# Kernel tuning notes

Hardware: AMD Instinct MI355X
Metric: run time of the kernel (lower is better)

The kernel has to match this reference:

```python
import jax, jax.numpy as jnp
import numpy as np

B, C, IMG, P = 64, 3, 224, 16
D, L, H, DH, M, NC = 768, 12, 12, 64, 3072, 1000
INNER = H * DH
PD = C * P * P          # patch_dim = 768
NP = (IMG // P) ** 2    # 196 patches


def setup_inputs() -> dict:
    key = jax.random.key(0)
    ks = jax.random.split(key, 16)
    s = 0.02
    nrm = lambda k, shape: jax.random.normal(k, shape, jnp.float32) * s
    return dict(
        img=jax.random.normal(ks[0], (B, C, IMG, IMG), jnp.float32),
        patch_ln1_g=jnp.ones(PD), patch_ln1_b=jnp.zeros(PD),
        patch_w=nrm(ks[1], (PD, D)), patch_b=jnp.zeros(D),
        patch_ln2_g=jnp.ones(D), patch_ln2_b=jnp.zeros(D),
        pos_emb=nrm(ks[2], (1, NP + 1, D)),
        cls_tok=nrm(ks[3], (1, 1, D)),
        attn_ln_g=jnp.ones((L, D)), attn_ln_b=jnp.zeros((L, D)),
        w_qkv=nrm(ks[4], (L, D, 3 * INNER)),
        w_out=nrm(ks[5], (L, INNER, D)), b_out=jnp.zeros((L, D)),
        ff_ln_g=jnp.ones((L, D)), ff_ln_b=jnp.zeros((L, D)),
        ff_w1=nrm(ks[6], (L, D, M)), ff_b1=jnp.zeros((L, M)),
        ff_w2=nrm(ks[7], (L, M, D)), ff_b2=jnp.zeros((L, D)),
        final_ln_g=jnp.ones(D), final_ln_b=jnp.zeros(D),
        head_w=nrm(ks[8], (D, NC)), head_b=jnp.zeros(NC),
    )


def _ln(x, g, b, eps=1e-5):
    m = x.mean(-1, keepdims=True)
    v = ((x - m) ** 2).mean(-1, keepdims=True)
    return (x - m) / jnp.sqrt(v + eps) * g + b


def reference(img, patch_ln1_g, patch_ln1_b, patch_w, patch_b, patch_ln2_g,
              patch_ln2_b, pos_emb, cls_tok, attn_ln_g, attn_ln_b, w_qkv,
              w_out, b_out, ff_ln_g, ff_ln_b, ff_w1, ff_b1, ff_w2, ff_b2,
              final_ln_g, final_ln_b, head_w, head_b):
    b, c, hh, ww = img.shape
    h, w = hh // P, ww // P
    # Rearrange 'b c (h p1) (w p2) -> b (h w) (p1 p2 c)'
    x = img.reshape(b, c, h, P, w, P).transpose(0, 2, 4, 3, 5, 1).reshape(b, h * w, P * P * c)
    x = _ln(x, patch_ln1_g, patch_ln1_b)
    x = x @ patch_w + patch_b
    x = _ln(x, patch_ln2_g, patch_ln2_b)
    n = x.shape[1]
    x = jnp.concatenate([jnp.broadcast_to(cls_tok, (b, 1, x.shape[-1])), x], axis=1)
    x = x + pos_emb[:, : n + 1]
    scale = DH ** -0.5
    for l in range(L):
        xn = _ln(x, attn_ln_g[l], attn_ln_b[l])
        qkv = xn @ w_qkv[l]  # [b, n+1, 3*inner]
        q, k, v = jnp.split(qkv, 3, axis=-1)
        sp = lambda t: t.reshape(b, -1, H, DH).transpose(0, 2, 1, 3)  # b h n d
        q, k, v = sp(q), sp(k), sp(v)
        # softmax variant: exp(scores*scale), normalize by sum + eps (no max-subtract, faithful to source)
        numer = jnp.exp(jnp.einsum('bhid,bhjd->bhij', q, k) * scale)
        attn = numer / (numer.sum(-1, keepdims=True) + 1e-8)
        out = jnp.einsum('bhij,bhjd->bhid', attn, v)
        out = out.transpose(0, 2, 1, 3).reshape(b, -1, INNER)
        x = out @ w_out[l] + b_out[l] + x
        xn = _ln(x, ff_ln_g[l], ff_ln_b[l])
        hid = jax.nn.gelu(xn @ ff_w1[l] + ff_b1[l], approximate=False)
        x = hid @ ff_w2[l] + ff_b2[l] + x
    x = _ln(x, final_ln_g, final_ln_b)
    return x[:, 0] @ head_w + head_b
```

## Files before the change

### kernel.cpp

```cpp
#include <hip/hip_runtime.h>
#include <hip/hip_bf16.h>
#include <math.h>

#define B_     64
#define NTOK   197
#define NPATCH 196
#define D768   768
#define NL     12
#define NH     12
#define MFF    3072
#define NCLS   1000
#define ROWS   (B_ * NTOK)
#define PROWS  (B_ * NPATCH)
#define ROWS_PAD 12672

typedef unsigned short ushort;
typedef __bf16 bf16x8 __attribute__((ext_vector_type(8)));
typedef float  f32x4  __attribute__((ext_vector_type(4)));
typedef unsigned short u16x4 __attribute__((ext_vector_type(4)));

__device__ __forceinline__ ushort f2b(float f) {
  __hip_bfloat16 h = __float2bfloat16(f);
  return *reinterpret_cast<ushort*>(&h);
}

__device__ __forceinline__ void gload16(const ushort* g, ushort* lds) {
  __builtin_amdgcn_global_load_lds((const __attribute__((address_space(1))) void*)g,
                                   (__attribute__((address_space(3))) void*)lds, 16, 0, 0);
}

__device__ __forceinline__ float gelu_f(float v) {
  float t = v * fmaf(0.0713548162726f, v * v, 1.5957691216f);
  return v / (1.0f + __expf(-t));
}

__device__ __forceinline__ void block_mean_rstd(float s, float sq, float& mean, float& rstd) {
#pragma unroll
  for (int off = 32; off; off >>= 1) { s += __shfl_xor(s, off); sq += __shfl_xor(sq, off); }
  __shared__ float ss[4], ssq[4];
  int w = threadIdx.x >> 6;
  if ((threadIdx.x & 63) == 0) { ss[w] = s; ssq[w] = sq; }
  __syncthreads();
  s  = ss[0] + ss[1] + ss[2] + ss[3];
  sq = ssq[0] + ssq[1] + ssq[2] + ssq[3];
  mean = s * (1.0f / 768.0f);
  float var = sq * (1.0f / 768.0f) - mean * mean;
  rstd = rsqrtf(var + 1e-5f);
}

__global__ __launch_bounds__(256) void ln_rows_b(const float* __restrict__ in, long in_stride,
                                                 const float* __restrict__ g,
                                                 const float* __restrict__ bta,
                                                 ushort* __restrict__ out) {
  const float* xr = in + (size_t)blockIdx.x * in_stride;
  int t = threadIdx.x;
  float v0 = xr[t], v1 = xr[t + 256], v2 = xr[t + 512];
  float mean, rstd;
  block_mean_rstd(v0 + v1 + v2, v0 * v0 + v1 * v1 + v2 * v2, mean, rstd);
  ushort* o = out + (size_t)blockIdx.x * 768;
  o[t]       = f2b((v0 - mean) * rstd * g[t]       + bta[t]);
  o[t + 256] = f2b((v1 - mean) * rstd * g[t + 256] + bta[t + 256]);
  o[t + 512] = f2b((v2 - mean) * rstd * g[t + 512] + bta[t + 512]);
}

__global__ __launch_bounds__(256) void patch_ln1(const float* __restrict__ img,
                                                 const float* __restrict__ g,
                                                 const float* __restrict__ bta,
                                                 ushort* __restrict__ xp) {
  int pidx = blockIdx.x;
  int b = pidx / NPATCH, hw = pidx % NPATCH;
  int ph = hw / 14, pw = hw % 14;
  int t = threadIdx.x;
  float v[3];
#pragma unroll
  for (int u = 0; u < 3; ++u) {
    int k = t + u * 256;
    int c = k % 3, p2 = (k / 3) & 15, p1 = k / 48;
    v[u] = img[(((size_t)b * 3 + c) * 224 + ph * 16 + p1) * 224 + pw * 16 + p2];
  }
  float mean, rstd;
  block_mean_rstd(v[0] + v[1] + v[2], v[0] * v[0] + v[1] * v[1] + v[2] * v[2], mean, rstd);
  ushort* o = xp + (size_t)pidx * 768;
#pragma unroll
  for (int u = 0; u < 3; ++u) { int k = t + u * 256; o[k] = f2b((v[u] - mean) * rstd * g[k] + bta[k]); }
}

__global__ __launch_bounds__(256) void ln2_pos(const float* __restrict__ xe,
                                               const float* __restrict__ g,
                                               const float* __restrict__ bta,
                                               const float* __restrict__ pos,
                                               float* __restrict__ x) {
  int pidx = blockIdx.x;
  int b = pidx / NPATCH, i = pidx % NPATCH;
  const float* xr = xe + (size_t)pidx * 768;
  int t = threadIdx.x;
  float v0 = xr[t], v1 = xr[t + 256], v2 = xr[t + 512];
  float mean, rstd;
  block_mean_rstd(v0 + v1 + v2, v0 * v0 + v1 * v1 + v2 * v2, mean, rstd);
  const float* p = pos + (size_t)(1 + i) * 768;
  float* o = x + ((size_t)b * NTOK + 1 + i) * 768;
  o[t]       = (v0 - mean) * rstd * g[t]       + bta[t]       + p[t];
  o[t + 256] = (v1 - mean) * rstd * g[t + 256] + bta[t + 256] + p[t + 256];
  o[t + 512] = (v2 - mean) * rstd * g[t + 512] + bta[t + 512] + p[t + 512];
}

__global__ __launch_bounds__(256) void cls_init(const float* __restrict__ cls_tok,
                                                const float* __restrict__ pos,
                                                float* __restrict__ x) {
  int b = blockIdx.x, t = threadIdx.x;
  float* o = x + (size_t)b * NTOK * 768;
#pragma unroll
  for (int u = 0; u < 3; ++u) { int k = t + u * 256; o[k] = cls_tok[k] + pos[k]; }
}

__global__ __launch_bounds__(256) void transpose_cast(const float* __restrict__ W,
                                                      ushort* __restrict__ Wt,
                                                      int K, int N) {
  __shared__ float t[32][33];
  int n0 = blockIdx.x * 32, k0 = blockIdx.y * 32;
  int tx = threadIdx.x, ty = threadIdx.y;
#pragma unroll
  for (int u = 0; u < 32; u += 8) {
    int n = n0 + tx;
    t[ty + u][tx] = (n < N) ? W[(size_t)(k0 + ty + u) * N + n] : 0.f;
  }
  __syncthreads();
#pragma unroll
  for (int u = 0; u < 32; u += 8) {
    int n = n0 + ty + u;
    if (n < N) Wt[(size_t)n * K + k0 + tx] = f2b(t[tx][ty + u]);
  }
}

__global__ __launch_bounds__(256) void transpose4(const float* __restrict__ wq,
                                                  const float* __restrict__ wo,
                                                  const float* __restrict__ w1,
                                                  const float* __restrict__ w2,
                                                  ushort* __restrict__ tq,
                                                  ushort* __restrict__ to,
                                                  ushort* __restrict__ t1,
                                                  ushort* __restrict__ t2) {
  int bid = blockIdx.x;
  const float* W; ushort* Wt; int K, N, xt;
  if (bid < 1728)      {             W = wq; Wt = tq; K = 768;  N = 2304; xt = 72; }
  else if (bid < 2304) { bid -= 1728; W = wo; Wt = to; K = 768;  N = 768;  xt = 24; }
  else if (bid < 4608) { bid -= 2304; W = w1; Wt = t1; K = 768;  N = 3072; xt = 96; }
  else                 { bid -= 4608; W = w2; Wt = t2; K = 3072; N = 768;  xt = 24; }
  int n0 = (bid % xt) * 32, k0 = (bid / xt) * 32;
  __shared__ float t[32][33];
  int tx = threadIdx.x, ty = threadIdx.y;
#pragma unroll
  for (int u = 0; u < 32; u += 8)
    t[ty + u][tx] = W[(size_t)(k0 + ty + u) * N + n0 + tx];
  __syncthreads();
#pragma unroll
  for (int u = 0; u < 32; u += 8)
    Wt[(size_t)(n0 + ty + u) * K + k0 + tx] = f2b(t[tx][ty + u]);
}

template<int EP, int RESID, int OBF>
__global__ __launch_bounds__(256, 4) void gemm_v6(const ushort* __restrict__ A,
                                                  const ushort* __restrict__ Bt,
                                                  const float* __restrict__ bias,
                                                  const float* __restrict__ resid,
                                                  void* __restrict__ Cv,
                                                  int M, int N, int K) {
  __shared__ ushort smem[2 * 8192];

  const int tid = threadIdx.x;
  const int w = tid >> 6, l = tid & 63;
  const int fr = l & 15, fc = l >> 4;

  const int ntx = gridDim.x;
  const int nwg = ntx * gridDim.y;
  const int orig = blockIdx.y * ntx + blockIdx.x;
  const int q = nwg >> 3, r = nwg & 7, xcd = orig & 7, idx = orig >> 3;
  const int wg = (xcd < r ? xcd * (q + 1) : r * (q + 1) + (xcd - r) * q) + idx;
  const int row0 = (wg / ntx) * 128, col0 = (wg % ntx) * 128;

  const int wr = (w >> 1) * 64, wc = (w & 1) * 64;

  const int srow = tid >> 2;
  const int sg = (tid & 3) ^ ((srow >> 1) & 3);
  const ushort* pA0 = A  + (size_t)(row0 + srow) * K + sg * 8;
  const ushort* pA1 = A  + (size_t)(row0 + 64 + srow) * K + sg * 8;
  const ushort* pB0 = Bt + (size_t)(col0 + srow) * K + sg * 8;
  const ushort* pB1 = Bt + (size_t)(col0 + 64 + srow) * K + sg * 8;

  auto stage = [&](int t_, ushort* dst) {
    const int k0 = t_ * 32;
    gload16(pA0 + k0, dst + tid * 8);
    gload16(pA1 + k0, dst + (tid + 256) * 8);
    gload16(pB0 + k0, dst + 4096 + tid * 8);
    gload16(pB1 + k0, dst + 4096 + (tid + 256) * 8);
  };

  int idxA[4], idxB[4];
#pragma unroll
  for (int m = 0; m < 4; ++m) {
    int rA = wr + m * 16 + fr;
    idxA[m] = rA * 32 + ((fc ^ ((rA >> 1) & 3)) << 3);
  }
#pragma unroll
  for (int n = 0; n < 4; ++n) {
    int rB = wc + n * 16 + fr;
    idxB[n] = rB * 32 + ((fc ^ ((rB >> 1) & 3)) << 3);
  }

  f32x4 acc[4][4] = {};

  auto compute = [&](const ushort* As) {
    const ushort* Bs = As + 4096;
    bf16x8 a_[4], b_[4];
#pragma unroll
    for (int m = 0; m < 4; ++m) a_[m] = *(const bf16x8*)(As + idxA[m]);
#pragma unroll
    for (int n = 0; n < 4; ++n) b_[n] = *(const bf16x8*)(Bs + idxB[n]);
#pragma unroll
    for (int m = 0; m < 4; ++m)
#pragma unroll
      for (int n = 0; n < 4; ++n)
        acc[m][n] = __builtin_amdgcn_mfma_f32_16x16x32_bf16(b_[n], a_[m], acc[m][n], 0, 0, 0);
  };

#define VM4() asm volatile("s_waitcnt vmcnt(4)" ::: "memory")
#define VM0() asm volatile("s_waitcnt vmcnt(0)" ::: "memory")

  const int NT = K >> 5;

  stage(0, smem);
  for (int t = 0; t < NT; t += 2) {
    if (t + 1 < NT) { stage(t + 1, smem + 8192); VM4(); } else VM0();
    __builtin_amdgcn_s_barrier();
    compute(smem);
    __builtin_amdgcn_s_barrier();
    if (t + 1 < NT) {
      if (t + 2 < NT) { stage(t + 2, smem); VM4(); } else VM0();
      __builtin_amdgcn_s_barrier();
      compute(smem + 8192);
      __builtin_amdgcn_s_barrier();
    }
  }
#undef VM4
#undef VM0

  if (!OBF) {
    float* Cf = (float*)Cv;
#pragma unroll
    for (int m = 0; m < 4; ++m) {
      int row = row0 + wr + m * 16 + fr;
      if (row >= M) continue;
#pragma unroll
      for (int n = 0; n < 4; ++n) {
        int col = col0 + wc + n * 16 + fc * 4;
        f32x4 v = acc[m][n];
        if (bias) v += *(const f32x4*)(bias + col);
        if (EP) {
#pragma unroll
          for (int rr = 0; rr < 4; ++rr) v[rr] = gelu_f(v[rr]);
        }
        if (RESID) v += *(const f32x4*)(resid + (size_t)row * N + col);
        *(f32x4*)(Cf + (size_t)row * N + col) = v;
      }
    }
  } else {
    __syncthreads();
    ushort* Cw = smem + w * 4096;
#pragma unroll
    for (int m = 0; m < 4; ++m) {
      int rl = m * 16 + fr;
#pragma unroll
      for (int n = 0; n < 4; ++n) {
        int col = col0 + wc + n * 16 + fc * 4;
        f32x4 v = acc[m][n];
        if (bias) v += *(const f32x4*)(bias + col);
        if (EP) {
#pragma unroll
          for (int rr = 0; rr < 4; ++rr) v[rr] = gelu_f(v[rr]);
        }
        u16x4 pk = { f2b(v[0]), f2b(v[1]), f2b(v[2]), f2b(v[3]) };
        int s = (n * 4 + fc) ^ (rl & 7);
        *(u16x4*)(Cw + rl * 64 + s * 4) = pk;
      }
    }
    ushort* Cb = (ushort*)Cv;
#pragma unroll
    for (int pp = 0; pp < 16; ++pp) {
      int rl = pp * 4 + (l >> 4);
      int cs = l & 15;
      u16x4 pk = *(const u16x4*)(Cw + rl * 64 + ((cs ^ (rl & 7)) * 4));
      int row = row0 + wr + rl;
      if (row < M) *(u16x4*)(Cb + (size_t)row * N + col0 + wc + cs * 4) = pk;
    }
  }
}

template<int EP, int RESID, int OBF>
__global__ __launch_bounds__(256) void gemm_bt(const ushort* __restrict__ A,
                                               const ushort* __restrict__ Bt,
                                               const float* __restrict__ bias,
                                               const float* __restrict__ resid,
                                               void* __restrict__ C,
                                               int M, int N, int K) {
  __shared__ ushort As[128 * 32];
  __shared__ ushort Bs[128 * 32];
  int tid = threadIdx.x;
  int w = tid >> 6, l = tid & 63;
  int fr = l & 15, fc = l >> 4;
  int row0 = blockIdx.y * 128, col0 = blockIdx.x * 128;
  int wr = (w >> 1) * 64, wc = (w & 1) * 64;

  int srow0 = w * 32 + (l >> 2);
  int srow1 = srow0 + 16;
  int sc0 = (((l & 3) ^ ((srow0 >> 1) & 3)) << 3);
  int sc1 = (((l & 3) ^ ((srow1 >> 1) & 3)) << 3);
  const ushort* ga0 = A  + (size_t)(row0 + srow0) * K + sc0;
  const ushort* ga1 = A  + (size_t)(row0 + srow1) * K + sc1;
  const ushort* gb0 = Bt + (size_t)(col0 + srow0) * K + sc0;
  const ushort* gb1 = Bt + (size_t)(col0 + srow1) * K + sc1;

  int idxA[4], idxB[4];
#pragma unroll
  for (int m = 0; m < 4; ++m) {
    int rA = wr + m * 16 + fr;
    idxA[m] = rA * 32 + ((fc ^ ((rA >> 1) & 3)) << 3);
  }
#pragma unroll
  for (int n = 0; n < 4; ++n) {
    int rB = wc + n * 16 + fr;
    idxB[n] = rB * 32 + ((fc ^ ((rB >> 1) & 3)) << 3);
  }

  f32x4 acc[4][4] = {};

  for (int k0 = 0; k0 < K; k0 += 32) {
    gload16(ga0 + k0, &As[w * 1024]);
    gload16(ga1 + k0, &As[w * 1024 + 512]);
    gload16(gb0 + k0, &Bs[w * 1024]);
    gload16(gb1 + k0, &Bs[w * 1024 + 512]);
    __syncthreads();
    bf16x8 af[4], bfr[4];
#pragma unroll
    for (int m = 0; m < 4; ++m) af[m] = *(const bf16x8*)(As + idxA[m]);
#pragma unroll
    for (int n = 0; n < 4; ++n) bfr[n] = *(const bf16x8*)(Bs + idxB[n]);
#pragma unroll
    for (int m = 0; m < 4; ++m)
#pragma unroll
      for (int n = 0; n < 4; ++n)
        acc[m][n] = __builtin_amdgcn_mfma_f32_16x16x32_bf16(af[m], bfr[n], acc[m][n], 0, 0, 0);
    __syncthreads();
  }

#pragma unroll
  for (int n = 0; n < 4; ++n) {
    int col = col0 + wc + n * 16 + fr;
    if (col >= N) continue;
    float bv = bias ? bias[col] : 0.f;
#pragma unroll
    for (int m = 0; m < 4; ++m) {
#pragma unroll
      for (int rr = 0; rr < 4; ++rr) {
        int row = row0 + wr + m * 16 + fc * 4 + rr;
        if (row >= M) continue;
        float v = acc[m][n][rr] + bv;
        if (EP == 1) v = 0.5f * v * (1.0f + erff(v * 0.70710678118654752f));
        if (RESID) v += resid[(size_t)row * N + col];
        if (OBF) ((ushort*)C)[(size_t)row * N + col] = f2b(v);
        else     ((float*)C)[(size_t)row * N + col]  = v;
      }
    }
  }
}

__global__ __launch_bounds__(256) void attn_mfma(const ushort* __restrict__ qkv,
                                                 ushort* __restrict__ aout) {
  int bid = blockIdx.x;
  int qt = bid & 3;
  int h  = (bid >> 2) % NH;
  int b  = (bid >> 2) / NH;
  int tid = threadIdx.x, w = tid >> 6, l = tid & 63;
  int fr = l & 15, fc = l >> 4;

  __shared__ ushort Vt[64 * 64];
  __shared__ ushort Pl[4 * 16 * 64];

  const size_t brow = (size_t)b * NTOK;
  int q0 = qt * 64 + w * 16;

  bf16x8 qf[2];
  {
    const ushort* qp = qkv + (brow + q0 + fr) * 2304 + h * 64 + fc * 8;
    qf[0] = *(const bf16x8*)qp;
    qf[1] = *(const bf16x8*)(qp + 32);
  }
  float rs[4] = {0.f, 0.f, 0.f, 0.f};
  f32x4 oc[4] = {};

  for (int kt = 0; kt < 4; ++kt) {
    __syncthreads();
    {
      int key = tid >> 2, d0 = (tid & 3) * 16;
      int j = kt * 64 + key;
      bool valid = j < NTOK;
      const ushort* vp = qkv + (brow + j) * 2304 + 1536 + h * 64 + d0;
      ushort vbuf[16];
      if (valid) {
        *(bf16x8*)(vbuf)     = *(const bf16x8*)vp;
        *(bf16x8*)(vbuf + 8) = *(const bf16x8*)(vp + 8);
      } else {
#pragma unroll
        for (int i = 0; i < 16; ++i) vbuf[i] = 0;
      }
#pragma unroll
      for (int i = 0; i < 16; ++i) {
        int d = d0 + i;
        int byte = d * 128 + ((((key >> 3)) ^ (d & 7)) << 4) + (key & 7) * 2;
        Vt[byte >> 1] = vbuf[i];
      }
    }
    f32x4 sc[4];
#pragma unroll
    for (int n = 0; n < 4; ++n) {
      f32x4 z = {};
      const ushort* kp = qkv + (brow + kt * 64 + n * 16 + fr) * 2304 + 768 + h * 64 + fc * 8;
      bf16x8 k0 = *(const bf16x8*)kp;
      bf16x8 k1 = *(const bf16x8*)(kp + 32);
      z = __builtin_amdgcn_mfma_f32_16x16x32_bf16(qf[0], k0, z, 0, 0, 0);
      z = __builtin_amdgcn_mfma_f32_16x16x32_bf16(qf[1], k1, z, 0, 0, 0);
      sc[n] = z;
    }
    float part[4] = {0.f, 0.f, 0.f, 0.f};
#pragma unroll
    for (int n = 0; n < 4; ++n) {
      int j = kt * 64 + n * 16 + fr;
      bool jv = j < NTOK;
#pragma unroll
      for (int rr = 0; rr < 4; ++rr) {
        float e = jv ? __expf(sc[n][rr] * 0.125f) : 0.f;
        part[rr] += e;
        int row = fc * 4 + rr, col = n * 16 + fr;
        int byte = row * 128 + (((col >> 3) ^ (row & 7)) << 4) + (col & 7) * 2;
        Pl[w * 1024 + (byte >> 1)] = f2b(e);
      }
    }
#pragma unroll
    for (int rr = 0; rr < 4; ++rr) {
      float p = part[rr];
      p += __shfl_xor(p, 1); p += __shfl_xor(p, 2);
      p += __shfl_xor(p, 4); p += __shfl_xor(p, 8);
      rs[rr] += p;
    }
    __syncthreads();
#pragma unroll
    for (int ks = 0; ks < 2; ++ks) {
      int prow = fr;
      int pbyte = prow * 128 + (((ks * 4 + fc) ^ (prow & 7)) << 4);
      bf16x8 pf = *(const bf16x8*)(Pl + w * 1024 + (pbyte >> 1));
#pragma unroll
      for (int n = 0; n < 4; ++n) {
        int d = n * 16 + fr;
        int vb = d * 128 + (((ks * 4 + fc) ^ (d & 7)) << 4);
        bf16x8 vf = *(const bf16x8*)(Vt + (vb >> 1));
        oc[n] = __builtin_amdgcn_mfma_f32_16x16x32_bf16(pf, vf, oc[n], 0, 0, 0);
      }
    }
  }
#pragma unroll
  for (int n = 0; n < 4; ++n) {
#pragma unroll
    for (int rr = 0; rr < 4; ++rr) {
      int qq = q0 + fc * 4 + rr;
      if (qq < NTOK) {
        float v = oc[n][rr] / (rs[rr] + 1e-8f);
        aout[(brow + qq) * 768 + h * 64 + n * 16 + fr] = f2b(v);
      }
    }
  }
}

extern "C" void kernel_launch(void* const* d_in, const int* in_sizes, int n_in,
                              void* d_out, int out_size, void* d_ws, size_t ws_size,
                              hipStream_t stream) {
  const float* img       = (const float*)d_in[0];
  const float* p_ln1_g   = (const float*)d_in[1];
  const float* p_ln1_b   = (const float*)d_in[2];
  const float* patch_w   = (const float*)d_in[3];
  const float* patch_b   = (const float*)d_in[4];
  const float* p_ln2_g   = (const float*)d_in[5];
  const float* p_ln2_b   = (const float*)d_in[6];
  const float* pos_emb   = (const float*)d_in[7];
  const float* cls_tok   = (const float*)d_in[8];
  const float* attn_ln_g = (const float*)d_in[9];
  const float* attn_ln_b = (const float*)d_in[10];
  const float* w_qkv     = (const float*)d_in[11];
  const float* w_out     = (const float*)d_in[12];
  const float* b_out     = (const float*)d_in[13];
  const float* ff_ln_g   = (const float*)d_in[14];
  const float* ff_ln_b   = (const float*)d_in[15];
  const float* ff_w1     = (const float*)d_in[16];
  const float* ff_b1     = (const float*)d_in[17];
  const float* ff_w2     = (const float*)d_in[18];
  const float* ff_b2     = (const float*)d_in[19];
  const float* fin_ln_g  = (const float*)d_in[20];
  const float* fin_ln_b  = (const float*)d_in[21];
  const float* head_w    = (const float*)d_in[22];
  const float* head_b    = (const float*)d_in[23];
  float* out = (float*)d_out;

  char* p = (char*)d_ws;
  auto alloc = [&](size_t bytes) { char* r = p; p += (bytes + 255) & ~(size_t)255; return r; };
  float*  x      = (float*) alloc((size_t)ROWS_PAD * 768 * 4);
  ushort* xnb    = (ushort*)alloc((size_t)ROWS_PAD * 768 * 2);
  ushort* qkvb   = (ushort*)alloc((size_t)ROWS_PAD * 2304 * 2);
  ushort* aoutb  = (ushort*)alloc((size_t)ROWS_PAD * 768 * 2);
  ushort* wtq    = (ushort*)alloc((size_t)2304 * 768 * 2);
  ushort* wto    = (ushort*)alloc((size_t)768 * 768 * 2);
  ushort* wt1    = (ushort*)alloc((size_t)3072 * 768 * 2);
  ushort* wt2    = (ushort*)alloc((size_t)768 * 3072 * 2);
  ushort* pwt    = (ushort*)alloc((size_t)768 * 768 * 2);
  ushort* hwt    = (ushort*)alloc((size_t)1024 * 768 * 2);
  ushort* xclsb  = (ushort*)alloc((size_t)128 * 768 * 2);
  ushort* hidb   = qkvb;
  ushort* xpb    = xnb;
  float*  xe     = (float*)qkvb;

  dim3 blk(256), tblk(32, 8);

  transpose_cast<<<dim3(24, 24), tblk, 0, stream>>>(patch_w, pwt, 768, 768);
  transpose_cast<<<dim3(32, 24), tblk, 0, stream>>>(head_w, hwt, 768, 1000);
  patch_ln1<<<PROWS, blk, 0, stream>>>(img, p_ln1_g, p_ln1_b, xpb);
  gemm_v6<0, 0, 0><<<dim3(6, 98), blk, 0, stream>>>(xpb, pwt, patch_b, nullptr, xe,
                                                    PROWS, 768, 768);
  ln2_pos<<<PROWS, blk, 0, stream>>>(xe, p_ln2_g, p_ln2_b, pos_emb, x);
  cls_init<<<B_, blk, 0, stream>>>(cls_tok, pos_emb, x);

  for (int l = 0; l < NL; ++l) {
    transpose4<<<6912, tblk, 0, stream>>>(w_qkv + (size_t)l * 768 * 2304,
                                          w_out + (size_t)l * 768 * 768,
                                          ff_w1 + (size_t)l * 768 * MFF,
                                          ff_w2 + (size_t)l * MFF * 768,
                                          wtq, wto, wt1, wt2);

    ln_rows_b<<<ROWS, blk, 0, stream>>>(x, 768, attn_ln_g + (size_t)l * 768,
                                        attn_ln_b + (size_t)l * 768, xnb);
    gemm_v6<0, 0, 1><<<dim3(18, 99), blk, 0, stream>>>(xnb, wtq, nullptr, nullptr, qkvb,
                                                       ROWS, 2304, 768);
    attn_mfma<<<B_ * NH * 4, blk, 0, stream>>>(qkvb, aoutb);
    gemm_v6<0, 1, 0><<<dim3(6, 99), blk, 0, stream>>>(aoutb, wto, b_out + (size_t)l * 768,
                                                      x, x, ROWS, 768, 768);
    ln_rows_b<<<ROWS, blk, 0, stream>>>(x, 768, ff_ln_g + (size_t)l * 768,
                                        ff_ln_b + (size_t)l * 768, xnb);
    gemm_v6<1, 0, 1><<<dim3(24, 99), blk, 0, stream>>>(xnb, wt1, ff_b1 + (size_t)l * MFF,
                                                       nullptr, hidb, ROWS, MFF, 768);
    gemm_v6<0, 1, 0><<<dim3(6, 99), blk, 0, stream>>>(hidb, wt2, ff_b2 + (size_t)l * 768,
                                                      x, x, ROWS, 768, MFF);
  }

  ln_rows_b<<<B_, blk, 0, stream>>>(x, (long)NTOK * 768, fin_ln_g, fin_ln_b, xclsb);
  gemm_bt<0, 0, 0><<<dim3(8, 1), blk, 0, stream>>>(xclsb, hwt, head_b, nullptr, out,
                                                   B_, NCLS, 768);
}
```

Measured before the change: 4.344 ms.

## Widen GEMM tiles to 128x256 and pre-transpose all layer weights once

```diff
diff --git a/kernel.cpp b/kernel.cpp
--- a/kernel.cpp
+++ b/kernel.cpp
@@ -132,6 +132,28 @@
   }
 }
 
+__device__ __forceinline__ void transpose_layer(int bid,
+                                                const float* wq, const float* wo,
+                                                const float* w1, const float* w2,
+                                                ushort* tq, ushort* to,
+                                                ushort* t1, ushort* t2) {
+  const float* W; ushort* Wt; int K, N, xt;
+  if (bid < 1728)      {             W = wq; Wt = tq; K = 768;  N = 2304; xt = 72; }
+  else if (bid < 2304) { bid -= 1728; W = wo; Wt = to; K = 768;  N = 768;  xt = 24; }
+  else if (bid < 4608) { bid -= 2304; W = w1; Wt = t1; K = 768;  N = 3072; xt = 96; }
+  else                 { bid -= 4608; W = w2; Wt = t2; K = 3072; N = 768;  xt = 24; }
+  int n0 = (bid % xt) * 32, k0 = (bid / xt) * 32;
+  __shared__ float t[32][33];
+  int tx = threadIdx.x, ty = threadIdx.y;
+#pragma unroll
+  for (int u = 0; u < 32; u += 8)
+    t[ty + u][tx] = W[(size_t)(k0 + ty + u) * N + n0 + tx];
+  __syncthreads();
+#pragma unroll
+  for (int u = 0; u < 32; u += 8)
+    Wt[(size_t)(n0 + ty + u) * K + k0 + tx] = f2b(t[tx][ty + u]);
+}
+
 __global__ __launch_bounds__(256) void transpose4(const float* __restrict__ wq,
                                                   const float* __restrict__ wo,
                                                   const float* __restrict__ w1,
@@ -140,32 +162,33 @@
                                                   ushort* __restrict__ to,
                                                   ushort* __restrict__ t1,
                                                   ushort* __restrict__ t2) {
-  int bid = blockIdx.x;
-  const float* W; ushort* Wt; int K, N, xt;
-  if (bid < 1728)      {             W = wq; Wt = tq; K = 768;  N = 2304; xt = 72; }
-  else if (bid < 2304) { bid -= 1728; W = wo; Wt = to; K = 768;  N = 768;  xt = 24; }
-  else if (bid < 4608) { bid -= 2304; W = w1; Wt = t1; K = 768;  N = 3072; xt = 96; }
-  else                 { bid -= 4608; W = w2; Wt = t2; K = 3072; N = 768;  xt = 24; }
-  int n0 = (bid % xt) * 32, k0 = (bid / xt) * 32;
-  __shared__ float t[32][33];
-  int tx = threadIdx.x, ty = threadIdx.y;
-#pragma unroll
-  for (int u = 0; u < 32; u += 8)
-    t[ty + u][tx] = W[(size_t)(k0 + ty + u) * N + n0 + tx];
-  __syncthreads();
-#pragma unroll
-  for (int u = 0; u < 32; u += 8)
-    Wt[(size_t)(n0 + ty + u) * K + k0 + tx] = f2b(t[tx][ty + u]);
+  transpose_layer(blockIdx.x, wq, wo, w1, w2, tq, to, t1, t2);
+}
+
+__global__ __launch_bounds__(256) void transpose_all(const float* __restrict__ wq,
+                                                     const float* __restrict__ wo,
+                                                     const float* __restrict__ w1,
+                                                     const float* __restrict__ w2,
+                                                     ushort* __restrict__ tq,
+                                                     ushort* __restrict__ to,
+                                                     ushort* __restrict__ t1,
+                                                     ushort* __restrict__ t2) {
+  int l = blockIdx.x / 6912, bid = blockIdx.x % 6912;
+  transpose_layer(bid,
+                  wq + (size_t)l * 768 * 2304, wo + (size_t)l * 768 * 768,
+                  w1 + (size_t)l * 768 * MFF,  w2 + (size_t)l * MFF * 768,
+                  tq + (size_t)l * 2304 * 768, to + (size_t)l * 768 * 768,
+                  t1 + (size_t)l * MFF * 768,  t2 + (size_t)l * 768 * MFF);
 }
 
 template<int EP, int RESID, int OBF>
-__global__ __launch_bounds__(256, 4) void gemm_v6(const ushort* __restrict__ A,
+__global__ __launch_bounds__(256, 2) void gemm_v7(const ushort* __restrict__ A,
                                                   const ushort* __restrict__ Bt,
                                                   const float* __restrict__ bias,
                                                   const float* __restrict__ resid,
                                                   void* __restrict__ Cv,
                                                   int M, int N, int K) {
-  __shared__ ushort smem[2 * 8192];
+  __shared__ ushort smem[2 * 12288];
 
   const int tid = threadIdx.x;
   const int w = tid >> 6, l = tid & 63;
@@ -176,9 +199,9 @@
   const int orig = blockIdx.y * ntx + blockIdx.x;
   const int q = nwg >> 3, r = nwg & 7, xcd = orig & 7, idx = orig >> 3;
   const int wg = (xcd < r ? xcd * (q + 1) : r * (q + 1) + (xcd - r) * q) + idx;
-  const int row0 = (wg / ntx) * 128, col0 = (wg % ntx) * 128;
-
-  const int wr = (w >> 1) * 64, wc = (w & 1) * 64;
+  const int row0 = (wg / ntx) * 128, col0 = (wg % ntx) * 256;
+
+  const int wrow = (w >> 1) * 64, wcol = (w & 1) * 128;
 
   const int srow = tid >> 2;
   const int sg = (tid & 3) ^ ((srow >> 1) & 3);
@@ -186,73 +209,78 @@
   const ushort* pA1 = A  + (size_t)(row0 + 64 + srow) * K + sg * 8;
   const ushort* pB0 = Bt + (size_t)(col0 + srow) * K + sg * 8;
   const ushort* pB1 = Bt + (size_t)(col0 + 64 + srow) * K + sg * 8;
+  const ushort* pB2 = Bt + (size_t)(col0 + 128 + srow) * K + sg * 8;
+  const ushort* pB3 = Bt + (size_t)(col0 + 192 + srow) * K + sg * 8;
 
   auto stage = [&](int t_, ushort* dst) {
     const int k0 = t_ * 32;
     gload16(pA0 + k0, dst + tid * 8);
     gload16(pA1 + k0, dst + (tid + 256) * 8);
-    gload16(pB0 + k0, dst + 4096 + tid * 8);
-    gload16(pB1 + k0, dst + 4096 + (tid + 256) * 8);
+    ushort* db = dst + 4096;
+    gload16(pB0 + k0, db + tid * 8);
+    gload16(pB1 + k0, db + (tid + 256) * 8);
+    gload16(pB2 + k0, db + (tid + 512) * 8);
+    gload16(pB3 + k0, db + (tid + 768) * 8);
   };
 
-  int idxA[4], idxB[4];
+  int idxA[4], idxB[8];
 #pragma unroll
   for (int m = 0; m < 4; ++m) {
-    int rA = wr + m * 16 + fr;
+    int rA = wrow + m * 16 + fr;
     idxA[m] = rA * 32 + ((fc ^ ((rA >> 1) & 3)) << 3);
   }
 #pragma unroll
-  for (int n = 0; n < 4; ++n) {
-    int rB = wc + n * 16 + fr;
+  for (int n = 0; n < 8; ++n) {
+    int rB = wcol + n * 16 + fr;
     idxB[n] = rB * 32 + ((fc ^ ((rB >> 1) & 3)) << 3);
   }
 
-  f32x4 acc[4][4] = {};
+  f32x4 acc[4][8] = {};
 
   auto compute = [&](const ushort* As) {
     const ushort* Bs = As + 4096;
-    bf16x8 a_[4], b_[4];
+    bf16x8 a_[4], b_[8];
 #pragma unroll
     for (int m = 0; m < 4; ++m) a_[m] = *(const bf16x8*)(As + idxA[m]);
 #pragma unroll
-    for (int n = 0; n < 4; ++n) b_[n] = *(const bf16x8*)(Bs + idxB[n]);
+    for (int n = 0; n < 8; ++n) b_[n] = *(const bf16x8*)(Bs + idxB[n]);
 #pragma unroll
     for (int m = 0; m < 4; ++m)
 #pragma unroll
-      for (int n = 0; n < 4; ++n)
+      for (int n = 0; n < 8; ++n)
         acc[m][n] = __builtin_amdgcn_mfma_f32_16x16x32_bf16(b_[n], a_[m], acc[m][n], 0, 0, 0);
   };
 
-#define VM4() asm volatile("s_waitcnt vmcnt(4)" ::: "memory")
+#define VM6() asm volatile("s_waitcnt vmcnt(6)" ::: "memory")
 #define VM0() asm volatile("s_waitcnt vmcnt(0)" ::: "memory")
 
   const int NT = K >> 5;
 
   stage(0, smem);
   for (int t = 0; t < NT; t += 2) {
-    if (t + 1 < NT) { stage(t + 1, smem + 8192); VM4(); } else VM0();
+    if (t + 1 < NT) { stage(t + 1, smem + 12288); VM6(); } else VM0();
     __builtin_amdgcn_s_barrier();
     compute(smem);
     __builtin_amdgcn_s_barrier();
     if (t + 1 < NT) {
-      if (t + 2 < NT) { stage(t + 2, smem); VM4(); } else VM0();
+      if (t + 2 < NT) { stage(t + 2, smem); VM6(); } else VM0();
       __builtin_amdgcn_s_barrier();
-      compute(smem + 8192);
+      compute(smem + 12288);
       __builtin_amdgcn_s_barrier();
     }
   }
-#undef VM4
+#undef VM6
 #undef VM0
 
   if (!OBF) {
     float* Cf = (float*)Cv;
 #pragma unroll
     for (int m = 0; m < 4; ++m) {
-      int row = row0 + wr + m * 16 + fr;
+      int row = row0 + wrow + m * 16 + fr;
       if (row >= M) continue;
 #pragma unroll
-      for (int n = 0; n < 4; ++n) {
-        int col = col0 + wc + n * 16 + fc * 4;
+      for (int n = 0; n < 8; ++n) {
+        int col = col0 + wcol + n * 16 + fc * 4;
         f32x4 v = acc[m][n];
         if (bias) v += *(const f32x4*)(bias + col);
         if (EP) {
@@ -264,33 +292,38 @@
       }
     }
   } else {
-    __syncthreads();
     ushort* Cw = smem + w * 4096;
-#pragma unroll
-    for (int m = 0; m < 4; ++m) {
-      int rl = m * 16 + fr;
-#pragma unroll
-      for (int n = 0; n < 4; ++n) {
-        int col = col0 + wc + n * 16 + fc * 4;
-        f32x4 v = acc[m][n];
-        if (bias) v += *(const f32x4*)(bias + col);
-        if (EP) {
-#pragma unroll
-          for (int rr = 0; rr < 4; ++rr) v[rr] = gelu_f(v[rr]);
+    ushort* Cb = (ushort*)Cv;
+#pragma unroll
+    for (int mp = 0; mp < 2; ++mp) {
+#pragma unroll
+      for (int m2 = 0; m2 < 2; ++m2) {
+        int m = mp * 2 + m2;
+        int rl = m2 * 16 + fr;
+#pragma unroll
+        for (int n = 0; n < 8; ++n) {
+          int col = col0 + wcol + n * 16 + fc * 4;
+          f32x4 v = acc[m][n];
+          if (bias) v += *(const f32x4*)(bias + col);
+          if (EP) {
+#pragma unroll
+            for (int rr = 0; rr < 4; ++rr) v[rr] = gelu_f(v[rr]);
+          }
+          u16x4 pk = { f2b(v[0]), f2b(v[1]), f2b(v[2]), f2b(v[3]) };
+          int s = (n * 4 + fc) ^ (rl & 7);
+          *(u16x4*)(Cw + rl * 128 + s * 4) = pk;
         }
-        u16x4 pk = { f2b(v[0]), f2b(v[1]), f2b(v[2]), f2b(v[3]) };
-        int s = (n * 4 + fc) ^ (rl & 7);
-        *(u16x4*)(Cw + rl * 64 + s * 4) = pk;
-      }
-    }
-    ushort* Cb = (ushort*)Cv;
-#pragma unroll
-    for (int pp = 0; pp < 16; ++pp) {
-      int rl = pp * 4 + (l >> 4);
-      int cs = l & 15;
-      u16x4 pk = *(const u16x4*)(Cw + rl * 64 + ((cs ^ (rl & 7)) * 4));
-      int row = row0 + wr + rl;
-      if (row < M) *(u16x4*)(Cb + (size_t)row * N + col0 + wc + cs * 4) = pk;
+      }
+      asm volatile("s_waitcnt lgkmcnt(0)" ::: "memory");
+#pragma unroll
+      for (int pp = 0; pp < 16; ++pp) {
+        int rl = pp * 2 + (l >> 5);
+        int cs = l & 31;
+        u16x4 pk = *(const u16x4*)(Cw + rl * 128 + ((cs ^ (rl & 7)) * 4));
+        int row = row0 + wrow + mp * 32 + rl;
+        if (row < M) *(u16x4*)(Cb + (size_t)row * N + col0 + wcol + cs * 4) = pk;
+      }
+      asm volatile("s_waitcnt lgkmcnt(0)" ::: "memory");
     }
   }
 }
@@ -514,10 +547,6 @@
   ushort* xnb    = (ushort*)alloc((size_t)ROWS_PAD * 768 * 2);
   ushort* qkvb   = (ushort*)alloc((size_t)ROWS_PAD * 2304 * 2);
   ushort* aoutb  = (ushort*)alloc((size_t)ROWS_PAD * 768 * 2);
-  ushort* wtq    = (ushort*)alloc((size_t)2304 * 768 * 2);
-  ushort* wto    = (ushort*)alloc((size_t)768 * 768 * 2);
-  ushort* wt1    = (ushort*)alloc((size_t)3072 * 768 * 2);
-  ushort* wt2    = (ushort*)alloc((size_t)768 * 3072 * 2);
   ushort* pwt    = (ushort*)alloc((size_t)768 * 768 * 2);
   ushort* hwt    = (ushort*)alloc((size_t)1024 * 768 * 2);
   ushort* xclsb  = (ushort*)alloc((size_t)128 * 768 * 2);
@@ -525,35 +554,52 @@
   ushort* xpb    = xnb;
   float*  xe     = (float*)qkvb;
 
+  const size_t SQ = (size_t)2304 * 768, SO = (size_t)768 * 768, S1 = (size_t)MFF * 768;
+  size_t used = (size_t)(p - (char*)d_ws);
+  bool oneshot = (used + 12 * (SQ + SO + 2 * S1) * 2 + 4096) <= ws_size;
+  int nw = oneshot ? 12 : 1;
+  ushort* wtq = (ushort*)alloc(nw * SQ * 2);
+  ushort* wto = (ushort*)alloc(nw * SO * 2);
+  ushort* wt1 = (ushort*)alloc(nw * S1 * 2);
+  ushort* wt2 = (ushort*)alloc(nw * S1 * 2);
+
   dim3 blk(256), tblk(32, 8);
 
   transpose_cast<<<dim3(24, 24), tblk, 0, stream>>>(patch_w, pwt, 768, 768);
   transpose_cast<<<dim3(32, 24), tblk, 0, stream>>>(head_w, hwt, 768, 1000);
+  if (oneshot)
+    transpose_all<<<12 * 6912, tblk, 0, stream>>>(w_qkv, w_out, ff_w1, ff_w2,
+                                                  wtq, wto, wt1, wt2);
   patch_ln1<<<PROWS, blk, 0, stream>>>(img, p_ln1_g, p_ln1_b, xpb);
-  gemm_v6<0, 0, 0><<<dim3(6, 98), blk, 0, stream>>>(xpb, pwt, patch_b, nullptr, xe,
+  gemm_v7<0, 0, 0><<<dim3(3, 98), blk, 0, stream>>>(xpb, pwt, patch_b, nullptr, xe,
                                                     PROWS, 768, 768);
   ln2_pos<<<PROWS, blk, 0, stream>>>(xe, p_ln2_g, p_ln2_b, pos_emb, x);
   cls_init<<<B_, blk, 0, stream>>>(cls_tok, pos_emb, x);
 
   for (int l = 0; l < NL; ++l) {
-    transpose4<<<6912, tblk, 0, stream>>>(w_qkv + (size_t)l * 768 * 2304,
-                                          w_out + (size_t)l * 768 * 768,
-                                          ff_w1 + (size_t)l * 768 * MFF,
-                                          ff_w2 + (size_t)l * MFF * 768,
-                                          wtq, wto, wt1, wt2);
+    ushort* tq = wtq + (oneshot ? (size_t)l * SQ : 0);
+    ushort* to = wto + (oneshot ? (size_t)l * SO : 0);
+    ushort* t1 = wt1 + (oneshot ? (size_t)l * S1 : 0);
+    ushort* t2 = wt2 + (oneshot ? (size_t)l * S1 : 0);
+    if (!oneshot)
+      transpose4<<<6912, tblk, 0, stream>>>(w_qkv + (size_t)l * 768 * 2304,
+                                            w_out + (size_t)l * 768 * 768,
+                                            ff_w1 + (size_t)l * 768 * MFF,
+                                            ff_w2 + (size_t)l * MFF * 768,
+                                            tq, to, t1, t2);
 
     ln_rows_b<<<ROWS, blk, 0, stream>>>(x, 768, attn_ln_g + (size_t)l * 768,
                                         attn_ln_b + (size_t)l * 768, xnb);
-    gemm_v6<0, 0, 1><<<dim3(18, 99), blk, 0, stream>>>(xnb, wtq, nullptr, nullptr, qkvb,
-                                                       ROWS, 2304, 768);
+    gemm_v7<0, 0, 1><<<dim3(9, 99), blk, 0, stream>>>(xnb, tq, nullptr, nullptr, qkvb,
+                                                      ROWS, 2304, 768);
     attn_mfma<<<B_ * NH * 4, blk, 0, stream>>>(qkvb, aoutb);
-    gemm_v6<0, 1, 0><<<dim3(6, 99), blk, 0, stream>>>(aoutb, wto, b_out + (size_t)l * 768,
+    gemm_v7<0, 1, 0><<<dim3(3, 99), blk, 0, stream>>>(aoutb, to, b_out + (size_t)l * 768,
                                                       x, x, ROWS, 768, 768);
     ln_rows_b<<<ROWS, blk, 0, stream>>>(x, 768, ff_ln_g + (size_t)l * 768,
                                         ff_ln_b + (size_t)l * 768, xnb);
-    gemm_v6<1, 0, 1><<<dim3(24, 99), blk, 0, stream>>>(xnb, wt1, ff_b1 + (size_t)l * MFF,
+    gemm_v7<1, 0, 1><<<dim3(12, 99), blk, 0, stream>>>(xnb, t1, ff_b1 + (size_t)l * MFF,
                                                        nullptr, hidb, ROWS, MFF, 768);
-    gemm_v6<0, 1, 0><<<dim3(6, 99), blk, 0, stream>>>(hidb, wt2, ff_b2 + (size_t)l * 768,
+    gemm_v7<0, 1, 0><<<dim3(3, 99), blk, 0, stream>>>(hidb, t2, ff_b2 + (size_t)l * 768,
                                                       x, x, ROWS, 768, MFF);
   }
 
```

Result: slower. 4.612 ms (+6.2%).

## Store residual stream in bf16 and pre-transpose all layer weights in one launch

Applied to the files above, without the earlier changes.

```diff
diff --git a/kernel.cpp b/kernel.cpp
--- a/kernel.cpp
+++ b/kernel.cpp
@@ -23,6 +23,12 @@
   __hip_bfloat16 h = __float2bfloat16(f);
   return *reinterpret_cast<ushort*>(&h);
 }
+__device__ __forceinline__ float b2f(ushort u) {
+  unsigned int v = ((unsigned int)u) << 16;
+  float f;
+  __builtin_memcpy(&f, &v, 4);
+  return f;
+}
 
 __device__ __forceinline__ void gload16(const ushort* g, ushort* lds) {
   __builtin_amdgcn_global_load_lds((const __attribute__((address_space(1))) void*)g,
@@ -48,13 +54,13 @@
   rstd = rsqrtf(var + 1e-5f);
 }
 
-__global__ __launch_bounds__(256) void ln_rows_b(const float* __restrict__ in, long in_stride,
+__global__ __launch_bounds__(256) void ln_rows_b(const ushort* __restrict__ in, long in_stride,
                                                  const float* __restrict__ g,
                                                  const float* __restrict__ bta,
                                                  ushort* __restrict__ out) {
-  const float* xr = in + (size_t)blockIdx.x * in_stride;
+  const ushort* xr = in + (size_t)blockIdx.x * in_stride;
   int t = threadIdx.x;
-  float v0 = xr[t], v1 = xr[t + 256], v2 = xr[t + 512];
+  float v0 = b2f(xr[t]), v1 = b2f(xr[t + 256]), v2 = b2f(xr[t + 512]);
   float mean, rstd;
   block_mean_rstd(v0 + v1 + v2, v0 * v0 + v1 * v1 + v2 * v2, mean, rstd);
   ushort* o = out + (size_t)blockIdx.x * 768;
@@ -89,7 +95,7 @@
                                                const float* __restrict__ g,
                                                const float* __restrict__ bta,
                                                const float* __restrict__ pos,
-                                               float* __restrict__ x) {
+                                               ushort* __restrict__ x) {
   int pidx = blockIdx.x;
   int b = pidx / NPATCH, i = pidx % NPATCH;
   const float* xr = xe + (size_t)pidx * 768;
@@ -98,19 +104,19 @@
   float mean, rstd;
   block_mean_rstd(v0 + v1 + v2, v0 * v0 + v1 * v1 + v2 * v2, mean, rstd);
   const float* p = pos + (size_t)(1 + i) * 768;
-  float* o = x + ((size_t)b * NTOK + 1 + i) * 768;
-  o[t]       = (v0 - mean) * rstd * g[t]       + bta[t]       + p[t];
-  o[t + 256] = (v1 - mean) * rstd * g[t + 256] + bta[t + 256] + p[t + 256];
-  o[t + 512] = (v2 - mean) * rstd * g[t + 512] + bta[t + 512] + p[t + 512];
+  ushort* o = x + ((size_t)b * NTOK + 1 + i) * 768;
+  o[t]       = f2b((v0 - mean) * rstd * g[t]       + bta[t]       + p[t]);
+  o[t + 256] = f2b((v1 - mean) * rstd * g[t + 256] + bta[t + 256] + p[t + 256]);
+  o[t + 512] = f2b((v2 - mean) * rstd * g[t + 512] + bta[t + 512] + p[t + 512]);
 }
 
 __global__ __launch_bounds__(256) void cls_init(const float* __restrict__ cls_tok,
                                                 const float* __restrict__ pos,
-                                                float* __restrict__ x) {
+                                                ushort* __restrict__ x) {
   int b = blockIdx.x, t = threadIdx.x;
-  float* o = x + (size_t)b * NTOK * 768;
-#pragma unroll
-  for (int u = 0; u < 3; ++u) { int k = t + u * 256; o[k] = cls_tok[k] + pos[k]; }
+  ushort* o = x + (size_t)b * NTOK * 768;
+#pragma unroll
+  for (int u = 0; u < 3; ++u) { int k = t + u * 256; o[k] = f2b(cls_tok[k] + pos[k]); }
 }
 
 __global__ __launch_bounds__(256) void transpose_cast(const float* __restrict__ W,
@@ -130,6 +136,28 @@
     int n = n0 + ty + u;
     if (n < N) Wt[(size_t)n * K + k0 + tx] = f2b(t[tx][ty + u]);
   }
+}
+
+__device__ __forceinline__ void transpose_layer(int bid,
+                                                const float* wq, const float* wo,
+                                                const float* w1, const float* w2,
+                                                ushort* tq, ushort* to,
+                                                ushort* t1, ushort* t2) {
+  const float* W; ushort* Wt; int K, N, xt;
+  if (bid < 1728)      {             W = wq; Wt = tq; K = 768;  N = 2304; xt = 72; }
+  else if (bid < 2304) { bid -= 1728; W = wo; Wt = to; K = 768;  N = 768;  xt = 24; }
+  else if (bid < 4608) { bid -= 2304; W = w1; Wt = t1; K = 768;  N = 3072; xt = 96; }
+  else                 { bid -= 4608; W = w2; Wt = t2; K = 3072; N = 768;  xt = 24; }
+  int n0 = (bid % xt) * 32, k0 = (bid / xt) * 32;
+  __shared__ float t[32][33];
+  int tx = threadIdx.x, ty = threadIdx.y;
+#pragma unroll
+  for (int u = 0; u < 32; u += 8)
+    t[ty + u][tx] = W[(size_t)(k0 + ty + u) * N + n0 + tx];
+  __syncthreads();
+#pragma unroll
+  for (int u = 0; u < 32; u += 8)
+    Wt[(size_t)(n0 + ty + u) * K + k0 + tx] = f2b(t[tx][ty + u]);
 }
 
 __global__ __launch_bounds__(256) void transpose4(const float* __restrict__ wq,
@@ -140,29 +168,30 @@
                                                   ushort* __restrict__ to,
                                                   ushort* __restrict__ t1,
                                                   ushort* __restrict__ t2) {
-  int bid = blockIdx.x;
-  const float* W; ushort* Wt; int K, N, xt;
-  if (bid < 1728)      {             W = wq; Wt = tq; K = 768;  N = 2304; xt = 72; }
-  else if (bid < 2304) { bid -= 1728; W = wo; Wt = to; K = 768;  N = 768;  xt = 24; }
-  else if (bid < 4608) { bid -= 2304; W = w1; Wt = t1; K = 768;  N = 3072; xt = 96; }
-  else                 { bid -= 4608; W = w2; Wt = t2; K = 3072; N = 768;  xt = 24; }
-  int n0 = (bid % xt) * 32, k0 = (bid / xt) * 32;
-  __shared__ float t[32][33];
-  int tx = threadIdx.x, ty = threadIdx.y;
-#pragma unroll
-  for (int u = 0; u < 32; u += 8)
-    t[ty + u][tx] = W[(size_t)(k0 + ty + u) * N + n0 + tx];
-  __syncthreads();
-#pragma unroll
-  for (int u = 0; u < 32; u += 8)
-    Wt[(size_t)(n0 + ty + u) * K + k0 + tx] = f2b(t[tx][ty + u]);
+  transpose_layer(blockIdx.x, wq, wo, w1, w2, tq, to, t1, t2);
+}
+
+__global__ __launch_bounds__(256) void transpose_all(const float* __restrict__ wq,
+                                                     const float* __restrict__ wo,
+                                                     const float* __restrict__ w1,
+                                                     const float* __restrict__ w2,
+                                                     ushort* __restrict__ tq,
+                                                     ushort* __restrict__ to,
+                                                     ushort* __restrict__ t1,
+                                                     ushort* __restrict__ t2) {
+  int l = blockIdx.x / 6912, bid = blockIdx.x % 6912;
+  transpose_layer(bid,
+                  wq + (size_t)l * 768 * 2304, wo + (size_t)l * 768 * 768,
+                  w1 + (size_t)l * 768 * MFF,  w2 + (size_t)l * MFF * 768,
+                  tq + (size_t)l * 2304 * 768, to + (size_t)l * 768 * 768,
+                  t1 + (size_t)l * MFF * 768,  t2 + (size_t)l * 768 * MFF);
 }
 
 template<int EP, int RESID, int OBF>
 __global__ __launch_bounds__(256, 4) void gemm_v6(const ushort* __restrict__ A,
                                                   const ushort* __restrict__ Bt,
                                                   const float* __restrict__ bias,
-                                                  const float* __restrict__ resid,
+                                                  const void* __restrict__ resid,
                                                   void* __restrict__ Cv,
                                                   int M, int N, int K) {
   __shared__ ushort smem[2 * 8192];
@@ -259,7 +288,7 @@
 #pragma unroll
           for (int rr = 0; rr < 4; ++rr) v[rr] = gelu_f(v[rr]);
         }
-        if (RESID) v += *(const f32x4*)(resid + (size_t)row * N + col);
+        if (RESID) v += *(const f32x4*)((const float*)resid + (size_t)row * N + col);
         *(f32x4*)(Cf + (size_t)row * N + col) = v;
       }
     }
@@ -269,6 +298,7 @@
 #pragma unroll
     for (int m = 0; m < 4; ++m) {
       int rl = m * 16 + fr;
+      int row = row0 + wr + rl;
 #pragma unroll
       for (int n = 0; n < 4; ++n) {
         int col = col0 + wc + n * 16 + fc * 4;
@@ -277,6 +307,11 @@
         if (EP) {
 #pragma unroll
           for (int rr = 0; rr < 4; ++rr) v[rr] = gelu_f(v[rr]);
+        }
+        if (RESID) {
+          u16x4 rv = *(const u16x4*)((const ushort*)resid + (size_t)row * N + col);
+#pragma unroll
+          for (int rr = 0; rr < 4; ++rr) v[rr] += b2f(rv[rr]);
         }
         u16x4 pk = { f2b(v[0]), f2b(v[1]), f2b(v[2]), f2b(v[3]) };
         int s = (n * 4 + fc) ^ (rl & 7);
@@ -510,14 +545,10 @@
 
   char* p = (char*)d_ws;
   auto alloc = [&](size_t bytes) { char* r = p; p += (bytes + 255) & ~(size_t)255; return r; };
-  float*  x      = (float*) alloc((size_t)ROWS_PAD * 768 * 4);
+  ushort* x      = (ushort*)alloc((size_t)ROWS_PAD * 768 * 2);
   ushort* xnb    = (ushort*)alloc((size_t)ROWS_PAD * 768 * 2);
   ushort* qkvb   = (ushort*)alloc((size_t)ROWS_PAD * 2304 * 2);
   ushort* aoutb  = (ushort*)alloc((size_t)ROWS_PAD * 768 * 2);
-  ushort* wtq    = (ushort*)alloc((size_t)2304 * 768 * 2);
-  ushort* wto    = (ushort*)alloc((size_t)768 * 768 * 2);
-  ushort* wt1    = (ushort*)alloc((size_t)3072 * 768 * 2);
-  ushort* wt2    = (ushort*)alloc((size_t)768 * 3072 * 2);
   ushort* pwt    = (ushort*)alloc((size_t)768 * 768 * 2);
   ushort* hwt    = (ushort*)alloc((size_t)1024 * 768 * 2);
   ushort* xclsb  = (ushort*)alloc((size_t)128 * 768 * 2);
@@ -525,10 +556,22 @@
   ushort* xpb    = xnb;
   float*  xe     = (float*)qkvb;
 
+  const size_t SQ = (size_t)2304 * 768, SO = (size_t)768 * 768, S1 = (size_t)MFF * 768;
+  size_t used = (size_t)(p - (char*)d_ws);
+  bool oneshot = (used + 12 * (SQ + SO + 2 * S1) * 2 + 4096) <= ws_size;
+  int nw = oneshot ? 12 : 1;
+  ushort* wtq = (ushort*)alloc(nw * SQ * 2);
+  ushort* wto = (ushort*)alloc(nw * SO * 2);
+  ushort* wt1 = (ushort*)alloc(nw * S1 * 2);
+  ushort* wt2 = (ushort*)alloc(nw * S1 * 2);
+
   dim3 blk(256), tblk(32, 8);
 
   transpose_cast<<<dim3(24, 24), tblk, 0, stream>>>(patch_w, pwt, 768, 768);
   transpose_cast<<<dim3(32, 24), tblk, 0, stream>>>(head_w, hwt, 768, 1000);
+  if (oneshot)
+    transpose_all<<<12 * 6912, tblk, 0, stream>>>(w_qkv, w_out, ff_w1, ff_w2,
+                                                  wtq, wto, wt1, wt2);
   patch_ln1<<<PROWS, blk, 0, stream>>>(img, p_ln1_g, p_ln1_b, xpb);
   gemm_v6<0, 0, 0><<<dim3(6, 98), blk, 0, stream>>>(xpb, pwt, patch_b, nullptr, xe,
                                                     PROWS, 768, 768);
@@ -536,24 +579,29 @@
   cls_init<<<B_, blk, 0, stream>>>(cls_tok, pos_emb, x);
 
   for (int l = 0; l < NL; ++l) {
-    transpose4<<<6912, tblk, 0, stream>>>(w_qkv + (size_t)l * 768 * 2304,
-                                          w_out + (size_t)l * 768 * 768,
-                                          ff_w1 + (size_t)l * 768 * MFF,
-                                          ff_w2 + (size_t)l * MFF * 768,
-                                          wtq, wto, wt1, wt2);
+    ushort* tq = wtq + (oneshot ? (size_t)l * SQ : 0);
+    ushort* to = wto + (oneshot ? (size_t)l * SO : 0);
+    ushort* t1 = wt1 + (oneshot ? (size_t)l * S1 : 0);
+    ushort* t2 = wt2 + (oneshot ? (size_t)l * S1 : 0);
+    if (!oneshot)
+      transpose4<<<6912, tblk, 0, stream>>>(w_qkv + (size_t)l * 768 * 2304,
+                                            w_out + (size_t)l * 768 * 768,
+                                            ff_w1 + (size_t)l * 768 * MFF,
+                                            ff_w2 + (size_t)l * MFF * 768,
+                                            tq, to, t1, t2);
 
     ln_rows_b<<<ROWS, blk, 0, stream>>>(x, 768, attn_ln_g + (size_t)l * 768,
                                         attn_ln_b + (size_t)l * 768, xnb);
-    gemm_v6<0, 0, 1><<<dim3(18, 99), blk, 0, stream>>>(xnb, wtq, nullptr, nullptr, qkvb,
+    gemm_v6<0, 0, 1><<<dim3(18, 99), blk, 0, stream>>>(xnb, tq, nullptr, nullptr, qkvb,
                                                        ROWS, 2304, 768);
     attn_mfma<<<B_ * NH * 4, blk, 0, stream>>>(qkvb, aoutb);
-    gemm_v6<0, 1, 0><<<dim3(6, 99), blk, 0, stream>>>(aoutb, wto, b_out + (size_t)l * 768,
+    gemm_v6<0, 1, 1><<<dim3(6, 99), blk, 0, stream>>>(aoutb, to, b_out + (size_t)l * 768,
                                                       x, x, ROWS, 768, 768);
     ln_rows_b<<<ROWS, blk, 0, stream>>>(x, 768, ff_ln_g + (size_t)l * 768,
                                         ff_ln_b + (size_t)l * 768, xnb);
-    gemm_v6<1, 0, 1><<<dim3(24, 99), blk, 0, stream>>>(xnb, wt1, ff_b1 + (size_t)l * MFF,
+    gemm_v6<1, 0, 1><<<dim3(24, 99), blk, 0, stream>>>(xnb, t1, ff_b1 + (size_t)l * MFF,
                                                        nullptr, hidb, ROWS, MFF, 768);
-    gemm_v6<0, 1, 0><<<dim3(6, 99), blk, 0, stream>>>(hidb, wt2, ff_b2 + (size_t)l * 768,
+    gemm_v6<0, 1, 1><<<dim3(6, 99), blk, 0, stream>>>(hidb, t2, ff_b2 + (size_t)l * 768,
                                                       x, x, ROWS, 768, MFF);
   }
 
```

After: 4.228 ms. 1.03x faster.
